# Kernel tuning notes

Hardware: AMD Instinct MI355X
Metric: run time of the kernel (lower is better)

The kernel has to match this reference:

```python
import jax, jax.numpy as jnp
import numpy as np

EMB = 1024
HEADS = 16
HEAD_DIM = EMB // HEADS
EPS = 1e-5


def gelu_tanh(x):
    c = jnp.sqrt(jnp.asarray(2.0 / jnp.pi, x.dtype))
    return 0.5 * x * (1 + jnp.tanh(c * (x + 0.044715 * x ** 3)))


def layernorm(x, scale, shift):
    mean = jnp.mean(x, axis=-1, keepdims=True)
    var = jnp.mean((x - mean) ** 2, axis=-1, keepdims=True)
    return scale * (x - mean) / jnp.sqrt(var + EPS) + shift


def setup_inputs() -> dict:
    key = jax.random.key(0)
    ks = jax.random.split(key, 12)
    s = 0.02
    x = jax.random.normal(ks[0], (2, 2048, EMB), dtype=jnp.float32)
    Wq = jax.random.normal(ks[1], (EMB, EMB), dtype=jnp.float32) * s
    Wk = jax.random.normal(ks[2], (EMB, EMB), dtype=jnp.float32) * s
    Wv = jax.random.normal(ks[3], (EMB, EMB), dtype=jnp.float32) * s
    Wo = jax.random.normal(ks[4], (EMB, EMB), dtype=jnp.float32) * s
    bo = jnp.zeros((EMB,), jnp.float32)
    W1 = jax.random.normal(ks[5], (EMB, 4 * EMB), dtype=jnp.float32) * s
    b1 = jnp.zeros((4 * EMB,), jnp.float32)
    W2 = jax.random.normal(ks[6], (4 * EMB, EMB), dtype=jnp.float32) * s
    b2 = jnp.zeros((EMB,), jnp.float32)
    g1 = jnp.ones((EMB,), jnp.float32)
    s1 = jnp.zeros((EMB,), jnp.float32)
    g2 = jnp.ones((EMB,), jnp.float32)
    s2 = jnp.zeros((EMB,), jnp.float32)
    return {"x": x, "Wq": Wq, "Wk": Wk, "Wv": Wv, "Wo": Wo, "bo": bo,
            "W1": W1, "b1": b1, "W2": W2, "b2": b2,
            "g1": g1, "s1": s1, "g2": g2, "s2": s2}


def reference(x, Wq, Wk, Wv, Wo, bo, W1, b1, W2, b2, g1, s1, g2, s2):
    B, S, D = x.shape
    # --- attention sub-block (pre-LN) ---
    h = layernorm(x, g1, s1)
    q = (h @ Wq).reshape(B, S, HEADS, HEAD_DIM).transpose(0, 2, 1, 3)
    k = (h @ Wk).reshape(B, S, HEADS, HEAD_DIM).transpose(0, 2, 1, 3)
    v = (h @ Wv).reshape(B, S, HEADS, HEAD_DIM).transpose(0, 2, 1, 3)
    scores = jnp.einsum('bhqd,bhkd->bhqk', q, k) / jnp.sqrt(
        jnp.asarray(HEAD_DIM, x.dtype))
    causal = jnp.triu(jnp.ones((S, S), bool), k=1)
    scores = jnp.where(causal, -jnp.inf, scores)
    attn = jax.nn.softmax(scores, axis=-1)
    ctx = jnp.einsum('bhqk,bhkd->bhqd', attn, v)
    ctx = ctx.transpose(0, 2, 1, 3).reshape(B, S, D)
    x = x + (ctx @ Wo + bo)
    # --- FFN sub-block (pre-LN) ---
    h = layernorm(x, g2, s2)
    h = gelu_tanh(h @ W1 + b1) @ W2 + b2
    return x + h
```

## Files before the change

### kernel.cpp

```cpp
#include <hip/hip_runtime.h>
#include <hip/hip_bf16.h>
#include <math.h>
#include <stdint.h>

typedef __bf16 bf16;
typedef __bf16 bf16x2 __attribute__((ext_vector_type(2)));
typedef __bf16 bf16x4 __attribute__((ext_vector_type(4)));
typedef __bf16 bf16x8 __attribute__((ext_vector_type(8)));
typedef float f32x4 __attribute__((ext_vector_type(4)));
typedef float f32x16 __attribute__((ext_vector_type(16)));
typedef unsigned uint2v __attribute__((ext_vector_type(2)));
typedef unsigned uint4v __attribute__((ext_vector_type(4)));

#define MFMA16(a, b, c) __builtin_amdgcn_mfma_f32_16x16x32_bf16((a), (b), (c), 0, 0, 0)
#define MFMA32(a, b, c) __builtin_amdgcn_mfma_f32_32x32x16_bf16((a), (b), (c), 0, 0, 0)

constexpr int EMB = 1024;
constexpr int SEQ = 2048;
constexpr int BATCH = 2;
constexpr int NTOK = BATCH * SEQ;
constexpr int FFN = 4 * EMB;
constexpr int HEADS = 16;
constexpr int HDIM = 64;

#define QSCALE 0.18033688011112042f

__device__ __forceinline__ void gload16(const void* g, void* l) {
    __builtin_amdgcn_global_load_lds(
        (const __attribute__((address_space(1))) void*)g,
        (__attribute__((address_space(3))) void*)l,
        16, 0, 0);
}

__device__ __forceinline__ float xhalf_max(float x) {
    unsigned u = __float_as_uint(x);
    uint2v r = __builtin_amdgcn_permlane32_swap(u, u, false, false);
    return fmaxf(__uint_as_float(r[0]), __uint_as_float(r[1]));
}
__device__ __forceinline__ float xhalf_sum(float x) {
    unsigned u = __float_as_uint(x);
    uint2v r = __builtin_amdgcn_permlane32_swap(u, u, false, false);
    return __uint_as_float(r[0]) + __uint_as_float(r[1]);
}

__device__ __forceinline__ unsigned pkbf(float a, float b) {
    bf16x2 v;
    v[0] = (bf16)a;
    v[1] = (bf16)b;
    return __builtin_bit_cast(unsigned, v);
}

__global__ __launch_bounds__(256) void ln_kernel(const float* __restrict__ x,
                                                 const float* __restrict__ g,
                                                 const float* __restrict__ b,
                                                 bf16* __restrict__ out) {
    int row = blockIdx.x;
    int t = threadIdx.x;
    float4 v = reinterpret_cast<const float4*>(x + (size_t)row * EMB)[t];
    float s = v.x + v.y + v.z + v.w;
    float s2 = v.x * v.x + v.y * v.y + v.z * v.z + v.w * v.w;
#pragma unroll
    for (int o = 1; o < 64; o <<= 1) {
        s += __shfl_xor(s, o);
        s2 += __shfl_xor(s2, o);
    }
    __shared__ float ps[4], ps2[4];
    int w = t >> 6;
    if ((t & 63) == 0) { ps[w] = s; ps2[w] = s2; }
    __syncthreads();
    s = ps[0] + ps[1] + ps[2] + ps[3];
    s2 = ps2[0] + ps2[1] + ps2[2] + ps2[3];
    float mean = s * (1.f / EMB);
    float var = s2 * (1.f / EMB) - mean * mean;
    float rstd = rsqrtf(var + 1e-5f);
    float4 gv = reinterpret_cast<const float4*>(g)[t];
    float4 bv = reinterpret_cast<const float4*>(b)[t];
    bf16* op = out + (size_t)row * EMB + t * 4;
    op[0] = (bf16)(gv.x * (v.x - mean) * rstd + bv.x);
    op[1] = (bf16)(gv.y * (v.y - mean) * rstd + bv.y);
    op[2] = (bf16)(gv.z * (v.z - mean) * rstd + bv.z);
    op[3] = (bf16)(gv.w * (v.w - mean) * rstd + bv.w);
}

__global__ __launch_bounds__(256) void transpose_all(
    const float* __restrict__ Wq, const float* __restrict__ Wk,
    const float* __restrict__ Wv, const float* __restrict__ Wo,
    const float* __restrict__ W1, const float* __restrict__ W2,
    bf16* __restrict__ Wqkvt, bf16* __restrict__ Wot,
    bf16* __restrict__ W1t, bf16* __restrict__ W2t) {
    int b = blockIdx.x;
    const float* W;
    bf16* Wt;
    int K, N, tile;
    if (b < 4096) {
        int w = b >> 10;
        tile = b & 1023;
        W = (w == 0) ? Wq : (w == 1) ? Wk : (w == 2) ? Wv : Wo;
        Wt = (w == 3) ? Wot : Wqkvt + (size_t)w * EMB * EMB;
        K = EMB; N = EMB;
    } else if (b < 8192) {
        tile = b - 4096; W = W1; Wt = W1t; K = EMB; N = FFN;
    } else {
        tile = b - 8192; W = W2; Wt = W2t; K = FFN; N = EMB;
    }
    int ntx = N / 32;
    int n0 = (tile % ntx) * 32, k0 = (tile / ntx) * 32;
    __shared__ float tl[32][33];
    int tx = threadIdx.x & 31, ty = threadIdx.x >> 5;
#pragma unroll
    for (int i = 0; i < 4; i++)
        tl[ty + 8 * i][tx] = W[(size_t)(k0 + ty + 8 * i) * N + n0 + tx];
    __syncthreads();
#pragma unroll
    for (int i = 0; i < 4; i++)
        Wt[(size_t)(n0 + ty + 8 * i) * K + k0 + tx] = (bf16)tl[tx][ty + 8 * i];
}

__global__ __launch_bounds__(256) void vtrans(const bf16* __restrict__ v,
                                              bf16* __restrict__ vt) {
    int bh = blockIdx.y;
    int s0 = blockIdx.x * 64;
    const bf16* src = v + (size_t)bh * SEQ * HDIM + (size_t)s0 * HDIM;
    bf16* dst = vt + (size_t)bh * HDIM * SEQ + s0;
    __shared__ bf16 tile[64][72];
    int t = threadIdx.x;
    int s = t >> 2, d0 = (t & 3) * 16;
    bf16x8 a = *reinterpret_cast<const bf16x8*>(src + s * HDIM + d0);
    bf16x8 b = *reinterpret_cast<const bf16x8*>(src + s * HDIM + d0 + 8);
#pragma unroll
    for (int e = 0; e < 8; e++) {
        tile[d0 + e][s] = a[e];
        tile[d0 + 8 + e][s] = b[e];
    }
    __syncthreads();
    int d = t >> 2, c0 = (t & 3) * 16;
    bf16x8 o0 = *reinterpret_cast<const bf16x8*>(&tile[d][c0]);
    bf16x8 o1 = *reinterpret_cast<const bf16x8*>(&tile[d][c0 + 8]);
    *reinterpret_cast<bf16x8*>(dst + (size_t)d * SEQ + c0) = o0;
    *reinterpret_cast<bf16x8*>(dst + (size_t)d * SEQ + c0 + 8) = o1;
}

template <int MODE>
__global__ __launch_bounds__(512, 1) void gemm8p(const bf16* __restrict__ A,
                                                 const bf16* __restrict__ Bt,
                                                 int K, int N,
                                                 bf16* __restrict__ outB,
                                                 bf16* __restrict__ outB2,
                                                 const float* __restrict__ bias) {
    extern __shared__ char smem[];
    int t = threadIdx.x;
    int wave = t >> 6, lane = t & 63;
    int wr = wave >> 2, wc = wave & 3;
    int lr = lane & 15, lg = lane >> 4;
    int row0 = blockIdx.x * 256;
    int col0 = blockIdx.y * 256;

    int tilesAll = K / 64;
    int nz = gridDim.z, z = blockIdx.z;
    int base = tilesAll / nz, rem = tilesAll - base * nz;
    int myT = base + (z < rem ? 1 : 0);
    int tBeg = z * base + (z < rem ? z : rem);

    const char* aSrc[4];
    const char* bSrc[4];
#pragma unroll
    for (int i = 0; i < 4; i++) {
        int f = t + i * 512;
        int gr = f >> 3, gk = f & 7;
        aSrc[i] = (const char*)A + ((size_t)(row0 + gr) * K + ((gk ^ (gr & 7)) << 3)) * 2
                  + (size_t)tBeg * 128;
        bSrc[i] = (const char*)Bt + ((size_t)(col0 + gr) * K + ((gk ^ (gr & 7)) << 3)) * 2
                  + (size_t)tBeg * 128;
    }

    f32x4 acc[8][4];
#pragma unroll
    for (int m = 0; m < 8; m++)
#pragma unroll
        for (int n = 0; n < 4; n++) acc[m][n] = f32x4{0.f, 0.f, 0.f, 0.f};

#pragma unroll
    for (int i = 0; i < 4; i++) {
        gload16(aSrc[i], smem + (t + i * 512) * 16);
        gload16(bSrc[i], smem + 32768 + (t + i * 512) * 16);
    }
    __syncthreads();

    for (int tk = 0; tk < myT; tk++) {
        int cur = tk & 1;
        const char* la = smem + cur * 65536;
        const char* lb = la + 32768;
        char* na = smem + (cur ^ 1) * 65536;
        bool stage = (tk + 1 < myT);

        bf16x8 bfr[2][4];
#pragma unroll
        for (int ph = 0; ph < 4; ph++) {
            constexpr int PH_KH[4] = {0, 0, 1, 1};
            constexpr int PH_MH[4] = {0, 1, 0, 1};
            const int kh = PH_KH[ph], mh = PH_MH[ph];
            bf16x8 afr[4];
#pragma unroll
            for (int m = 0; m < 4; m++) {
                int row = wr * 128 + (mh * 4 + m) * 16 + lr;
                int gk = kh * 4 + lg;
                afr[m] = *reinterpret_cast<const bf16x8*>(
                    la + row * 128 + ((gk ^ (row & 7)) << 4));
            }
            if (mh == 0) {
#pragma unroll
                for (int n = 0; n < 4; n++) {
                    int row = wc * 64 + n * 16 + lr;
                    int gk = kh * 4 + lg;
                    bfr[kh][n] = *reinterpret_cast<const bf16x8*>(
                        lb + row * 128 + ((gk ^ (row & 7)) << 4));
                }
            }
            if (stage) {
                gload16(aSrc[ph] + 128, na + (t + ph * 512) * 16);
                gload16(bSrc[ph] + 128, na + 32768 + (t + ph * 512) * 16);
            }
            __builtin_amdgcn_s_barrier();
            __builtin_amdgcn_s_setprio(1);
#pragma unroll
            for (int m = 0; m < 4; m++)
#pragma unroll
                for (int n = 0; n < 4; n++)
                    acc[mh * 4 + m][n] = MFMA16(afr[m], bfr[kh][n], acc[mh * 4 + m][n]);
            __builtin_amdgcn_s_setprio(0);
            __builtin_amdgcn_s_barrier();
        }
#pragma unroll
        for (int i = 0; i < 4; i++) { aSrc[i] += 128; bSrc[i] += 128; }
        __syncthreads();
    }

    float bi[4];
    if (MODE == 2) {
#pragma unroll
        for (int n = 0; n < 4; n++) bi[n] = bias[col0 + wc * 64 + n * 16 + lr];
    }
    bf16* pd = outB;
    if (MODE == 3) pd = (z < 2) ? outB + (size_t)z * ((size_t)NTOK * EMB) : outB2;
#pragma unroll
    for (int mf = 0; mf < 8; mf++) {
#pragma unroll
        for (int r = 0; r < 4; r++) {
            int row = row0 + wr * 128 + mf * 16 + 4 * lg + r;
#pragma unroll
            for (int n = 0; n < 4; n++) {
                int col = col0 + wc * 64 + n * 16 + lr;
                float v = acc[mf][n][r];
                if (MODE == 0) {
                    int b_ = row >> 11, s_ = row & 2047;
                    int which = col >> 10, rem_ = col & 1023;
                    int h_ = rem_ >> 6, d_ = rem_ & 63;
                    float sc = (which == 0) ? QSCALE : 1.0f;
                    outB[(size_t)which * (NTOK * EMB) +
                         (((size_t)(b_ * HEADS + h_) * SEQ + s_) << 6) + d_] =
                        (bf16)(v * sc);
                } else if (MODE == 2) {
                    float u = v + bi[n];
                    float gl = 0.5f * u *
                               (1.f + tanhf(0.7978845608028654f *
                                            (u + 0.044715f * u * u * u)));
                    outB[(size_t)row * N + col] = (bf16)gl;
                } else {
                    pd[(size_t)row * N + col] = (bf16)v;
                }
            }
        }
    }
}

__global__ __launch_bounds__(256) void ffn2_reduce(const float* __restrict__ x1,
                                                   const bf16* __restrict__ p01,
                                                   const bf16* __restrict__ p2,
                                                   const float* __restrict__ bias,
                                                   float* __restrict__ out) {
    constexpr int UNITS = NTOK * EMB / 4;
    const bf16* p1 = p01 + (size_t)NTOK * EMB;
    for (int i = blockIdx.x * 256 + threadIdx.x; i < UNITS; i += gridDim.x * 256) {
        float4 r = reinterpret_cast<const float4*>(x1)[i];
        float4 bv = reinterpret_cast<const float4*>(bias)[i & (EMB / 4 - 1)];
        bf16x4 a0 = reinterpret_cast<const bf16x4*>(p01)[i];
        bf16x4 a1 = reinterpret_cast<const bf16x4*>(p1)[i];
        bf16x4 a2 = reinterpret_cast<const bf16x4*>(p2)[i];
        r.x += (float)a0[0] + (float)a1[0] + (float)a2[0] + bv.x;
        r.y += (float)a0[1] + (float)a1[1] + (float)a2[1] + bv.y;
        r.z += (float)a0[2] + (float)a1[2] + (float)a2[2] + bv.z;
        r.w += (float)a0[3] + (float)a1[3] + (float)a2[3] + bv.w;
        reinterpret_cast<float4*>(out)[i] = r;
    }
}

template <int BM, int BN, int BK, int MODE>
__global__ __launch_bounds__(256) void gemm_lds(const bf16* __restrict__ A,
                                                const bf16* __restrict__ Bt,
                                                int M, int N, int K,
                                                float* __restrict__ outF,
                                                bf16* __restrict__ outB,
                                                const float* __restrict__ bias,
                                                const float* __restrict__ resid) {
    constexpr int MR = BM / 32;
    constexpr int NR = BN / 32;
    constexpr int ACH = (BM * BK * 2) / 4096;
    constexpr int BCH = (BN * BK * 2) / 4096;
    __shared__ bf16 sA[BM * BK];
    __shared__ bf16 sB[BN * BK];
    int t = threadIdx.x;
    int wave = t >> 6, lane = t & 63;
    int wr = wave >> 1, wc = wave & 1;
    int lr = lane & 15, lg = lane >> 4;
    int row0 = blockIdx.x * BM;
    int col0 = blockIdx.y * BN;

    const char* aS[ACH];
    const char* bS[BCH];
#pragma unroll
    for (int c = 0; c < ACH; c++) {
        int o = (t + c * 256) * 16;
        aS[c] = (const char*)A + (size_t)(row0 + o / (2 * BK)) * K * 2 + (o & (2 * BK - 1));
    }
#pragma unroll
    for (int c = 0; c < BCH; c++) {
        int o = (t + c * 256) * 16;
        bS[c] = (const char*)Bt + (size_t)(col0 + o / (2 * BK)) * K * 2 + (o & (2 * BK - 1));
    }

    f32x4 acc[MR][NR];
#pragma unroll
    for (int m = 0; m < MR; m++)
#pragma unroll
        for (int n = 0; n < NR; n++) acc[m][n] = f32x4{0.f, 0.f, 0.f, 0.f};

    for (int k0 = 0; k0 < K; k0 += BK) {
        __syncthreads();
#pragma unroll
        for (int c = 0; c < ACH; c++)
            gload16(aS[c], (char*)sA + (t + c * 256) * 16);
#pragma unroll
        for (int c = 0; c < BCH; c++)
            gload16(bS[c], (char*)sB + (t + c * 256) * 16);
#pragma unroll
        for (int c = 0; c < ACH; c++) aS[c] += 2 * BK;
#pragma unroll
        for (int c = 0; c < BCH; c++) bS[c] += 2 * BK;
        __syncthreads();

#pragma unroll
        for (int ks = 0; ks < BK / 32; ks++) {
            bf16x8 a[MR], b[NR];
#pragma unroll
            for (int m = 0; m < MR; m++)
                a[m] = *reinterpret_cast<const bf16x8*>(
                    sA + (wr * (BM / 2) + m * 16 + lr) * BK + ks * 32 + 8 * lg);
#pragma unroll
            for (int n = 0; n < NR; n++)
                b[n] = *reinterpret_cast<const bf16x8*>(
                    sB + (wc * (BN / 2) + n * 16 + lr) * BK + ks * 32 + 8 * lg);
#pragma unroll
            for (int m = 0; m < MR; m++)
#pragma unroll
                for (int n = 0; n < NR; n++)
                    acc[m][n] = MFMA16(a[m], b[n], acc[m][n]);
        }
    }

#pragma unroll
    for (int m = 0; m < MR; m++) {
#pragma unroll
        for (int r = 0; r < 4; r++) {
            int row = row0 + wr * (BM / 2) + m * 16 + 4 * lg + r;
#pragma unroll
            for (int n = 0; n < NR; n++) {
                int col = col0 + wc * (BN / 2) + n * 16 + lr;
                float v = acc[m][n][r];
                size_t idx = (size_t)row * N + col;
                outF[idx] = resid[idx] + v + bias[col];
            }
        }
    }
}

__global__ __launch_bounds__(256, 3) void attn_kernel(const bf16* __restrict__ q,
                                                      const bf16* __restrict__ k,
                                                      const bf16* __restrict__ vt,
                                                      bf16* __restrict__ ctx) {
    int wg = blockIdx.x;
    int wgid = (wg & 7) * 64 + (wg >> 3);
    int bh = wgid >> 4;
    int pair = wgid & 15;
    const bf16* qh = q + (size_t)bh * SEQ * HDIM;
    const bf16* kh = k + (size_t)bh * SEQ * HDIM;
    const bf16* vh = vt + (size_t)bh * HDIM * SEQ;
    int t = threadIdx.x;
    int wave = t >> 6, lane = t & 63;
    int ql = lane & 31, hi = lane >> 5;

    int span = (wave < 2 ? (31 - pair) : pair) * 64;
    int qrow = span + (wave & 1) * 32;
    int myNc = span / 64 + 1;
    int ncAll = 32 - pair;

    __shared__ bf16 sK[2][64 * 64];
    __shared__ bf16 sV[2][64 * 64];

    int grow = t >> 3, gg = t & 7;
    const bf16* kSrc0 = kh + (size_t)grow * HDIM + ((gg ^ (grow & 7)) << 3);
    const bf16* kSrc1 = kh + (size_t)(grow + 32) * HDIM + ((gg ^ ((grow + 32) & 7)) << 3);
    const bf16* vSrc0 = vh + (size_t)grow * SEQ + ((gg ^ (grow & 7)) << 3);
    const bf16* vSrc1 = vh + (size_t)(grow + 32) * SEQ + ((gg ^ ((grow + 32) & 7)) << 3);
    char* kD0 = (char*)&sK[0][0] + wave * 1024;
    char* vD0 = (char*)&sV[0][0] + wave * 1024;

    int b_ = bh >> 4, h_ = bh & 15;

    bf16x8 qf[4];
#pragma unroll
    for (int ks = 0; ks < 4; ks++)
        qf[ks] = *reinterpret_cast<const bf16x8*>(
            qh + (size_t)(qrow + ql) * HDIM + ks * 16 + 8 * hi);

    f32x16 o0, o1;
#pragma unroll
    for (int r = 0; r < 16; r++) { o0[r] = 0.f; o1[r] = 0.f; }
    float mx = -1e30f, lsum = 0.f;

    gload16(kSrc0, kD0);
    gload16(kSrc1, kD0 + 4096);
    gload16(vSrc0, vD0);
    gload16(vSrc1, vD0 + 4096);
    __syncthreads();

    for (int c = 0; c < ncAll; c++) {
        int c0 = c * 64;
        if (c + 1 < ncAll) {
            int nb = (c + 1) & 1;
            int cn = c0 + 64;
            gload16(kSrc0 + (size_t)cn * HDIM, kD0 + nb * 8192);
            gload16(kSrc1 + (size_t)cn * HDIM, kD0 + nb * 8192 + 4096);
            gload16(vSrc0 + cn, vD0 + nb * 8192);
            gload16(vSrc1 + cn, vD0 + nb * 8192 + 4096);
        }

        if (c < myNc) {
            const char* kb_ = (const char*)&sK[c & 1][0];
            const char* vb_ = (const char*)&sV[c & 1][0];

            f32x16 st0, st1;
#pragma unroll
            for (int r = 0; r < 16; r++) { st0[r] = 0.f; st1[r] = 0.f; }
#pragma unroll
            for (int ks = 0; ks < 4; ks++) {
                int so = ((2 * ks + hi) ^ (ql & 7)) << 4;
                bf16x8 kA0 = *reinterpret_cast<const bf16x8*>(kb_ + ql * 128 + so);
                bf16x8 kA1 = *reinterpret_cast<const bf16x8*>(kb_ + (32 + ql) * 128 + so);
                st0 = MFMA32(kA0, qf[ks], st0);
                st1 = MFMA32(kA1, qf[ks], st1);
            }

            if (c == myNc - 1) {
#pragma unroll
                for (int r = 0; r < 16; r++) {
                    int kl = c0 + (r & 3) + 8 * (r >> 2) + 4 * hi;
                    if (kl > qrow + ql) st0[r] = -1e30f;
                    if (kl + 32 > qrow + ql) st1[r] = -1e30f;
                }
            }

            float pmax = -1e30f;
#pragma unroll
            for (int r = 0; r < 16; r++)
                pmax = fmaxf(pmax, fmaxf(st0[r], st1[r]));
            pmax = xhalf_max(pmax);
            float mxold = mx;
            bool defer = (pmax <= mxold + 8.0f);
            float mn = defer ? mxold : fmaxf(mxold, pmax);
            mx = mn;
            float ps = 0.f;
#pragma unroll
            for (int r = 0; r < 16; r++) {
                st0[r] = __builtin_amdgcn_exp2f(st0[r] - mn);
                st1[r] = __builtin_amdgcn_exp2f(st1[r] - mn);
                ps += st0[r] + st1[r];
            }
            ps = xhalf_sum(ps);
            if (!__all(defer)) {
                float scl = __builtin_amdgcn_exp2f(mxold - mn);
                lsum = lsum * scl + ps;
#pragma unroll
                for (int r = 0; r < 16; r++) { o0[r] *= scl; o1[r] *= scl; }
            } else {
                lsum += ps;
            }

#pragma unroll
            for (int h2 = 0; h2 < 2; h2++) {
                f32x16 P = h2 ? st1 : st0;
#pragma unroll
                for (int sub = 0; sub < 2; sub++) {
                    int ks = 2 * h2 + sub;
                    int bs = 8 * sub;
                    unsigned X0 = pkbf(P[bs + 0], P[bs + 1]);
                    unsigned X1 = pkbf(P[bs + 2], P[bs + 3]);
                    unsigned Y0 = pkbf(P[bs + 4], P[bs + 5]);
                    unsigned Y1 = pkbf(P[bs + 6], P[bs + 7]);
                    uint2v s0 = __builtin_amdgcn_permlane32_swap(X0, Y0, false, false);
                    uint2v s1 = __builtin_amdgcn_permlane32_swap(X1, Y1, false, false);
                    uint4v uw;
                    uw[0] = s0[0];
                    uw[1] = s1[0];
                    uw[2] = s0[1];
                    uw[3] = s1[1];
                    bf16x8 pb = __builtin_bit_cast(bf16x8, uw);
                    int so = ((2 * ks + hi) ^ (ql & 7)) << 4;
                    bf16x8 vA0 = *reinterpret_cast<const bf16x8*>(vb_ + ql * 128 + so);
                    bf16x8 vA1 = *reinterpret_cast<const bf16x8*>(vb_ + (32 + ql) * 128 + so);
                    o0 = MFMA32(vA0, pb, o0);
                    o1 = MFMA32(vA1, pb, o1);
                }
            }
        }

        __syncthreads();
    }

    float inv = 1.f / lsum;
    size_t base = ((size_t)b_ * SEQ + qrow + ql) * EMB + h_ * HDIM;
#pragma unroll
    for (int j = 0; j < 4; j++) {
        bf16x4 w0, w1;
#pragma unroll
        for (int e = 0; e < 4; e++) {
            w0[e] = (bf16)(o0[4 * j + e] * inv);
            w1[e] = (bf16)(o1[4 * j + e] * inv);
        }
        *reinterpret_cast<bf16x4*>(ctx + base + 8 * j + 4 * hi) = w0;
        *reinterpret_cast<bf16x4*>(ctx + base + 32 + 8 * j + 4 * hi) = w1;
    }
}

extern "C" void kernel_launch(void* const* d_in, const int* in_sizes, int n_in,
                              void* d_out, int out_size, void* d_ws, size_t ws_size,
                              hipStream_t stream) {
    const float* x  = (const float*)d_in[0];
    const float* Wq = (const float*)d_in[1];
    const float* Wk = (const float*)d_in[2];
    const float* Wv = (const float*)d_in[3];
    const float* Wo = (const float*)d_in[4];
    const float* bo = (const float*)d_in[5];
    const float* W1 = (const float*)d_in[6];
    const float* b1 = (const float*)d_in[7];
    const float* W2 = (const float*)d_in[8];
    const float* b2 = (const float*)d_in[9];
    const float* g1 = (const float*)d_in[10];
    const float* s1 = (const float*)d_in[11];
    const float* g2 = (const float*)d_in[12];
    const float* s2 = (const float*)d_in[13];

    const size_t MB = 1ull << 20;
    char* w = (char*)d_ws;
    bf16* Wqkvt = (bf16*)(w + 0 * MB);
    bf16* Wot = (bf16*)(w + 6 * MB);
    bf16* W1t = (bf16*)(w + 8 * MB);
    bf16* W2t = (bf16*)(w + 16 * MB);
    bf16* hbuf = (bf16*)(w + 24 * MB);
    bf16* vtb  = (bf16*)(w + 24 * MB);
    bf16* qkvb = (bf16*)(w + 32 * MB);
    bf16* qb   = (bf16*)(w + 32 * MB);
    bf16* kb   = (bf16*)(w + 40 * MB);
    bf16* vb   = (bf16*)(w + 48 * MB);
    bf16* ctxb = (bf16*)(w + 56 * MB);
    bf16* midb = (bf16*)(w + 32 * MB);
    float* x1  = (float*)(w + 64 * MB);
    bf16* p01  = (bf16*)(w + 0 * MB);
    bf16* p2   = (bf16*)(w + 24 * MB);

    hipFuncSetAttribute(reinterpret_cast<const void*>(gemm8p<0>),
                        hipFuncAttributeMaxDynamicSharedMemorySize, 131072);
    hipFuncSetAttribute(reinterpret_cast<const void*>(gemm8p<2>),
                        hipFuncAttributeMaxDynamicSharedMemorySize, 131072);
    hipFuncSetAttribute(reinterpret_cast<const void*>(gemm8p<3>),
                        hipFuncAttributeMaxDynamicSharedMemorySize, 131072);

    transpose_all<<<dim3(12288), 256, 0, stream>>>(Wq, Wk, Wv, Wo, W1, W2,
                                                   Wqkvt, Wot, W1t, W2t);

    ln_kernel<<<NTOK, 256, 0, stream>>>(x, g1, s1, hbuf);

    gemm8p<0><<<dim3(NTOK / 256, 3072 / 256), 512, 131072, stream>>>(
        hbuf, Wqkvt, EMB, 3072, qkvb, nullptr, nullptr);

    vtrans<<<dim3(SEQ / 64, BATCH * HEADS), 256, 0, stream>>>(vb, vtb);

    attn_kernel<<<dim3(512), 256, 0, stream>>>(qb, kb, vtb, ctxb);

    gemm_lds<128, 64, 32, 1><<<dim3(NTOK / 128, EMB / 64), 256, 0, stream>>>(
        ctxb, Wot, NTOK, EMB, EMB, x1, nullptr, bo, x);

    ln_kernel<<<NTOK, 256, 0, stream>>>(x1, g2, s2, hbuf);

    gemm8p<2><<<dim3(NTOK / 256, FFN / 256), 512, 131072, stream>>>(
        hbuf, W1t, EMB, FFN, midb, nullptr, b1);

    gemm8p<3><<<dim3(NTOK / 256, EMB / 256, 3), 512, 131072, stream>>>(
        midb, W2t, FFN, EMB, p01, p2, nullptr);
    ffn2_reduce<<<dim3(2048), 256, 0, stream>>>(x1, p01, p2, b2, (float*)d_out);
}
```

Measured before the change: 243.5 us.

## Reorder GEMM staging loads with partial vmcnt waits and cheaper exp2-based GELU

Restructures the GEMM's double-buffered global-to-LDS staging. B tiles are issued first and A tiles in an order matching the phases that consume them, and the full __syncthreads at the end of each k-step is replaced by partial s_waitcnt vmcnt(2) waits plus barriers, so compute can begin before every load has landed. Separately, the GELU epilogue replaces tanhf with an exp2-based sigmoid form (u/(1+exp(-2w))), which is algebraically equivalent and cheaper. The finer-grained waits depend on the exact order in which loads are issued and completed, so any mismatch between issue order and the vmcnt counts could race on the shared-memory buffer.

```diff
diff --git a/kernel.cpp b/kernel.cpp
--- a/kernel.cpp
+++ b/kernel.cpp
@@ -48,6 +48,12 @@
     v[0] = (bf16)a;
     v[1] = (bf16)b;
     return __builtin_bit_cast(unsigned, v);
+}
+
+__device__ __forceinline__ float gelu_f(float u) {
+    float w_ = 0.7978845608028654f * (u + 0.044715f * u * u * u);
+    float z = __builtin_amdgcn_exp2f(-2.8853900817779268f * w_);
+    return u / (1.f + z);
 }
 
 __global__ __launch_bounds__(256) void ln_kernel(const float* __restrict__ x,
@@ -179,12 +185,16 @@
 #pragma unroll
         for (int n = 0; n < 4; n++) acc[m][n] = f32x4{0.f, 0.f, 0.f, 0.f};
 
-#pragma unroll
-    for (int i = 0; i < 4; i++) {
-        gload16(aSrc[i], smem + (t + i * 512) * 16);
-        gload16(bSrc[i], smem + 32768 + (t + i * 512) * 16);
-    }
-    __syncthreads();
+    gload16(bSrc[0], smem + 32768 + (t + 0 * 512) * 16);
+    gload16(bSrc[1], smem + 32768 + (t + 1 * 512) * 16);
+    gload16(bSrc[2], smem + 32768 + (t + 2 * 512) * 16);
+    gload16(bSrc[3], smem + 32768 + (t + 3 * 512) * 16);
+    gload16(aSrc[0], smem + (t + 0 * 512) * 16);
+    gload16(aSrc[2], smem + (t + 2 * 512) * 16);
+    gload16(aSrc[1], smem + (t + 1 * 512) * 16);
+    gload16(aSrc[3], smem + (t + 3 * 512) * 16);
+    asm volatile("s_waitcnt vmcnt(2)" ::: "memory");
+    __builtin_amdgcn_s_barrier();
 
     for (int tk = 0; tk < myT; tk++) {
         int cur = tk & 1;
@@ -217,8 +227,19 @@
                 }
             }
             if (stage) {
-                gload16(aSrc[ph] + 128, na + (t + ph * 512) * 16);
-                gload16(bSrc[ph] + 128, na + 32768 + (t + ph * 512) * 16);
+                if (ph == 0) {
+                    gload16(bSrc[0] + 128, na + 32768 + (t + 0 * 512) * 16);
+                    gload16(bSrc[1] + 128, na + 32768 + (t + 1 * 512) * 16);
+                } else if (ph == 1) {
+                    gload16(bSrc[2] + 128, na + 32768 + (t + 2 * 512) * 16);
+                    gload16(bSrc[3] + 128, na + 32768 + (t + 3 * 512) * 16);
+                } else if (ph == 2) {
+                    gload16(aSrc[0] + 128, na + (t + 0 * 512) * 16);
+                    gload16(aSrc[2] + 128, na + (t + 2 * 512) * 16);
+                } else {
+                    gload16(aSrc[1] + 128, na + (t + 1 * 512) * 16);
+                    gload16(aSrc[3] + 128, na + (t + 3 * 512) * 16);
+                }
             }
             __builtin_amdgcn_s_barrier();
             __builtin_amdgcn_s_setprio(1);
@@ -228,11 +249,12 @@
                 for (int n = 0; n < 4; n++)
                     acc[mh * 4 + m][n] = MFMA16(afr[m], bfr[kh][n], acc[mh * 4 + m][n]);
             __builtin_amdgcn_s_setprio(0);
+            if (ph == 0 || ph == 3)
+                asm volatile("s_waitcnt vmcnt(2)" ::: "memory");
             __builtin_amdgcn_s_barrier();
         }
 #pragma unroll
         for (int i = 0; i < 4; i++) { aSrc[i] += 128; bSrc[i] += 128; }
-        __syncthreads();
     }
 
     float bi[4];
@@ -260,11 +282,7 @@
                          (((size_t)(b_ * HEADS + h_) * SEQ + s_) << 6) + d_] =
                         (bf16)(v * sc);
                 } else if (MODE == 2) {
-                    float u = v + bi[n];
-                    float gl = 0.5f * u *
-                               (1.f + tanhf(0.7978845608028654f *
-                                            (u + 0.044715f * u * u * u)));
-                    outB[(size_t)row * N + col] = (bf16)gl;
+                    outB[(size_t)row * N + col] = (bf16)gelu_f(v + bi[n]);
                 } else {
                     pd[(size_t)row * N + col] = (bf16)v;
                 }
```

New measurement: 233.1 us. 4.3% less time.
